# Optimization experiments

Hardware: AMD Instinct MI355X
Metric: run time of the kernel (lower is better)

Reference implementation:

```python
import jax, jax.numpy as jnp
import numpy as np

EPS = 1e-5


def layer_norm(x, g, b):
    m = jnp.mean(x, axis=-1, keepdims=True)
    v = jnp.mean((x - m) ** 2, axis=-1, keepdims=True)
    return (x - m) / jnp.sqrt(v + EPS) * g + b


def rel_shift(x, klen):
    # x: [q, p, b, n] -> Transformer-XL relative shift -> [q, klen, b, n]
    q, p, b, n = x.shape
    x = jnp.reshape(x, (p, q, b, n))
    x = x[1:]
    x = jnp.reshape(x, (q, p - 1, b, n))
    return x[:, :klen]


def setup_inputs() -> dict:
    S, B, D, NH, DH, DF = 1024, 4, 1024, 16, 64, 4096
    key = jax.random.key(0)
    ks = jax.random.split(key, 16)
    w = 0.02  # scale random params for numerical sanity
    return {
        "src": jax.random.normal(ks[0], (S, B, D), jnp.float32),
        "pos_emb": jax.random.normal(ks[1], (S + 1, B, D), jnp.float32),
        "src_mask": jnp.zeros((S, S), dtype=bool),
        "qw": jax.random.normal(ks[2], (D, NH, DH), jnp.float32) * w,
        "kw": jax.random.normal(ks[3], (D, NH, DH), jnp.float32) * w,
        "vw": jax.random.normal(ks[4], (D, NH, DH), jnp.float32) * w,
        "rw": jax.random.normal(ks[5], (D, NH, DH), jnp.float32) * w,
        "ow": jax.random.normal(ks[6], (D, NH, DH), jnp.float32) * w,
        "r_w_bias": jax.random.normal(ks[7], (NH, DH), jnp.float32) * w,
        "r_r_bias": jax.random.normal(ks[8], (NH, DH), jnp.float32) * w,
        "w1": jax.random.normal(ks[9], (DF, D), jnp.float32) * w,
        "b1": jnp.zeros((DF,), jnp.float32),
        "w2": jax.random.normal(ks[10], (D, DF), jnp.float32) * w,
        "b2": jnp.zeros((D,), jnp.float32),
        "g1": jnp.ones((D,), jnp.float32),
        "beta1": jnp.zeros((D,), jnp.float32),
        "g2": jnp.ones((D,), jnp.float32),
        "beta2": jnp.zeros((D,), jnp.float32),
    }


def reference(src, pos_emb, src_mask, qw, kw, vw, rw, ow, r_w_bias, r_r_bias,
              w1, b1, w2, b2, g1, beta1, g2, beta2):
    S = src.shape[0]
    d_head = qw.shape[-1]
    scale = 1.0 / d_head ** 0.5

    # mem=None -> cat == src; dropout layers are identity (eval)
    q_head = jnp.einsum('ibh,hnd->ibnd', src, qw)
    k_head = jnp.einsum('ibh,hnd->ibnd', src, kw)
    v_head = jnp.einsum('ibh,hnd->ibnd', src, vw)
    k_pos = jnp.einsum('ibh,hnd->ibnd', pos_emb, rw)

    ac = jnp.einsum('ibnd,jbnd->ijbn', q_head + r_w_bias, k_head)       # [S,S,B,N]
    bd = jnp.einsum('ibnd,jbnd->ijbn', q_head + r_r_bias, k_pos)        # [S,S+1,B,N]
    bd = rel_shift(bd, klen=S)

    mask = src_mask.astype(ac.dtype)[:, :, None, None]
    attn_score = (ac + bd) * scale - 1e30 * mask
    attn_prob = jax.nn.softmax(attn_score, axis=1)

    attn_vec = jnp.einsum('ijbn,jbnd->ibnd', attn_prob, v_head)
    attn_out = jnp.einsum('ibnd,hnd->ibh', attn_vec, ow)

    x = layer_norm(src + attn_out, g1, beta1)
    ff = jax.nn.gelu(x @ w1.T + b1, approximate=False) @ w2.T + b2
    return layer_norm(x + ff, g2, beta2)
```

## Files before the change

### kernel.cpp

```cpp
#include <hip/hip_runtime.h>
#include <math.h>

typedef __bf16 bf16x8 __attribute__((ext_vector_type(8)));
typedef __bf16 bf16x4 __attribute__((ext_vector_type(4)));
typedef float f32x4 __attribute__((ext_vector_type(4)));

__device__ __forceinline__ void gload_lds16(const __bf16* g, __bf16* l) {
  __builtin_amdgcn_global_load_lds((const __attribute__((address_space(1))) void*)g,
                                   (__attribute__((address_space(3))) void*)l, 16, 0, 0);
}

__device__ __forceinline__ float gelu_exact(float v) {
  return 0.5f * v * (1.f + erff(v * 0.70710678118654752f));
}

__global__ __launch_bounds__(256) void prep_all(
    const float* __restrict__ src, __bf16* __restrict__ srcB2,
    const float* __restrict__ pos, __bf16* __restrict__ posB,
    const float* __restrict__ ow, __bf16* __restrict__ owB,
    const float* __restrict__ w1, __bf16* __restrict__ w1B,
    const float* __restrict__ w2, __bf16* __restrict__ w2B,
    const float* __restrict__ qw, const float* __restrict__ kw,
    const float* __restrict__ vw, const float* __restrict__ rw,
    __bf16* __restrict__ qkvT, __bf16* __restrict__ rwT) {
  __shared__ float t[32][33];
  int bid = blockIdx.x;
  const int tid = threadIdx.x;
  if (bid < 4096) {
    const int i = bid & 1023, b = bid >> 10;
    const float4 v = *(const float4*)(src + ((size_t)(i * 4 + b)) * 1024 + tid * 4);
    bf16x4 o = {(__bf16)v.x, (__bf16)v.y, (__bf16)v.z, (__bf16)v.w};
    *(bf16x4*)(srcB2 + (size_t)bid * 1024 + tid * 4) = o;
    return;
  }
  bid -= 4096;
  if (bid < 3329) {
    const float* in; __bf16* out;
    if (bid < 1025) { in = pos; out = posB; }
    else if (bid < 1281) { bid -= 1025; in = ow; out = owB; }
    else if (bid < 2305) { bid -= 1281; in = w1; out = w1B; }
    else { bid -= 2305; in = w2; out = w2B; }
    const int base = bid * 4096 + tid * 4;
#pragma unroll
    for (int k2 = 0; k2 < 4; ++k2) {
      const int off = base + k2 * 1024;
      float4 v = *(const float4*)(in + off);
      bf16x4 o = {(__bf16)v.x, (__bf16)v.y, (__bf16)v.z, (__bf16)v.w};
      *(bf16x4*)(out + off) = o;
    }
    return;
  }
  bid -= 3329;
  const int z = bid >> 10, rem = bid & 1023;
  const float* in; __bf16* out;
  switch (z) {
    case 0: in = qw; out = qkvT; break;
    case 1: in = kw; out = qkvT + 1024 * 1024; break;
    case 2: in = vw; out = qkvT + 2048 * 1024; break;
    default: in = rw; out = rwT; break;
  }
  const int c0 = (rem & 31) * 32, r0 = (rem >> 5) * 32;
  const int tx = tid & 31, ty = tid >> 5;
  for (int yy = ty; yy < 32; yy += 8)
    t[yy][tx] = in[(size_t)(r0 + yy) * 1024 + c0 + tx];
  __syncthreads();
  for (int yy = ty; yy < 32; yy += 8)
    out[(size_t)(c0 + yy) * 1024 + r0 + tx] = (__bf16)t[tx][yy];
}

template<int BM, int BN, int MODE>
__device__ __forceinline__ void gemm_body(
    const __bf16* __restrict__ A, const __bf16* __restrict__ BT,
    float* __restrict__ Cf, __bf16* __restrict__ Cb,
    const float* __restrict__ bias, int M, int N, int K,
    int kStart, int kChunk, int mBase, int nBase, char* smemRaw) {
  constexpr int BK = 32;
  constexpr int ALOAD = (BM * BK) / 2048;
  constexpr int BLOAD = (BN * BK) / 2048;
  __bf16* lA = (__bf16*)smemRaw;
  __bf16* lB = (__bf16*)(smemRaw + 4 * BM * BK);
  const int tid = threadIdx.x;
  const int w = tid >> 6, l = tid & 63;
  const int lr = l & 15, lk = l >> 4;
  const int srow = tid >> 2;
  const int scol = (tid & 3) * 8;
  const int wbase = w * 512;

  const __bf16* aSrc[ALOAD];
  const __bf16* bSrc[BLOAD];
#pragma unroll
  for (int i = 0; i < ALOAD; ++i) {
    int grow = mBase + srow + i * 64;
    grow = grow < M ? grow : M - 1;
    aSrc[i] = A + (size_t)grow * K + kStart + scol;
  }
#pragma unroll
  for (int i = 0; i < BLOAD; ++i) {
    const int grow = nBase + srow + i * 64;
    bSrc[i] = BT + (size_t)grow * K + kStart + scol;
  }
  auto stage = [&](int buf) {
#pragma unroll
    for (int i = 0; i < ALOAD; ++i) {
      gload_lds16(aSrc[i], &lA[buf * BM * BK + i * 2048 + wbase]);
      aSrc[i] += BK;
    }
#pragma unroll
    for (int i = 0; i < BLOAD; ++i) {
      gload_lds16(bSrc[i], &lB[buf * BN * BK + i * 2048 + wbase]);
      bSrc[i] += BK;
    }
  };

  constexpr int WM = BM / 2, WN = BN / 2;
  constexpr int MF = WM / 16, NF = WN / 16;
  const int wr = w >> 1, wc = w & 1;
  f32x4 acc[MF][NF] = {};

  const int nIter = kChunk / BK;
  stage(0);
  int cur = 0;
#pragma unroll 1
  for (int t = 0; t < nIter; ++t) {
    __syncthreads();
    if (t + 1 < nIter) stage(cur ^ 1);
    bf16x8 af[MF], bfr[NF];
#pragma unroll
    for (int mi = 0; mi < MF; ++mi)
      af[mi] = *(const bf16x8*)&lA[cur * BM * BK + (wr * WM + mi * 16 + lr) * BK + lk * 8];
#pragma unroll
    for (int nj = 0; nj < NF; ++nj)
      bfr[nj] = *(const bf16x8*)&lB[cur * BN * BK + (wc * WN + nj * 16 + lr) * BK + lk * 8];
#pragma unroll
    for (int mi = 0; mi < MF; ++mi)
#pragma unroll
      for (int nj = 0; nj < NF; ++nj)
        acc[mi][nj] = __builtin_amdgcn_mfma_f32_16x16x32_bf16(af[mi], bfr[nj], acc[mi][nj], 0, 0, 0);
    cur ^= 1;
  }
#pragma unroll
  for (int mi = 0; mi < MF; ++mi) {
#pragma unroll
    for (int nj = 0; nj < NF; ++nj) {
      const int col = nBase + wc * WN + nj * 16 + lr;
      const int row0 = mBase + wr * WM + mi * 16 + lk * 4;
#pragma unroll
      for (int j = 0; j < 4; ++j) {
        const int row = row0 + j;
        if (row < M) {
          float v = acc[mi][nj][j];
          if constexpr (MODE == 1) {
            v = gelu_exact(v + bias[col]);
            Cb[(size_t)row * N + col] = (__bf16)v;
          } else if constexpr (MODE == 2) {
            Cb[(size_t)row * N + col] = (__bf16)v;
          } else {
            Cf[(size_t)row * N + col] = v;
          }
        }
      }
    }
  }
}

__global__ __launch_bounds__(256)
void proj2_kernel(const __bf16* __restrict__ vwT, const __bf16* __restrict__ srcB2,
                  const __bf16* __restrict__ posB, const __bf16* __restrict__ rwT,
                  __bf16* __restrict__ vTB, __bf16* __restrict__ kposB) {
  __shared__ __align__(16) char smem[4 * (128 + 64) * 32];
  const int raw = blockIdx.x;
  int bid = (raw & 7) * 130 + (raw >> 3);
  if (bid < 512) {
    gemm_body<128, 64, 2>(vwT, srcB2, nullptr, vTB, nullptr, 1024, 4096, 1024,
                          0, 1024, (bid >> 6) * 128, (bid & 63) * 64, smem);
  } else {
    const int t = bid - 512;
    gemm_body<128, 64, 2>(posB, rwT, nullptr, kposB, nullptr, 4100, 1024, 1024,
                          0, 1024, (t >> 4) * 128, (t & 15) * 64, smem);
  }
}

template<int MODE>
__global__ __launch_bounds__(512)
void gemm256(const __bf16* __restrict__ A, const __bf16* __restrict__ BT,
             __bf16* __restrict__ Cb, const float* __restrict__ bias,
             int M, int N, int K) {
  __shared__ __align__(16) __bf16 sm[3 * 24576];
  const int tid = threadIdx.x;
  const int wid = tid >> 6, l = tid & 63;
  const int lcol = l & 15, lk = l >> 4;
  const int wm = wid >> 1, wn = wid & 1;
  const int gx = gridDim.x;
  const int G = gx * gridDim.y;
  const int flat = blockIdx.y * gx + blockIdx.x;
  const int band = G >> 3;
  const int x8 = flat & 7, loc = flat >> 3;
  const int rpb = band / gx;
  const int ny = x8 * rpb + loc % rpb;
  const int nx = loc / rpb;
  const int mBase = ny * 256, nBase = nx * 128;

  int rowj[2], gslotj[2];
#pragma unroll
  for (int j = 0; j < 2; ++j) {
    const int u = (wid * 2 + j) * 64 + l;
    rowj[j] = u >> 3;
    gslotj[j] = (u & 7) ^ (rowj[j] & 7);
  }
  auto issueHT = [&](int kt, int ht, int side) {
    __bf16* base = sm + side * 24576 + (ht == 2 ? 16384 : ht * 8192);
#pragma unroll
    for (int j = 0; j < 2; ++j) {
      const __bf16* src = (ht < 2)
        ? A + (size_t)(mBase + ht * 128 + rowj[j]) * K + kt * 64 + gslotj[j] * 8
        : BT + (size_t)(nBase + rowj[j]) * K + kt * 64 + gslotj[j] * 8;
      gload_lds16(src, base + (wid * 2 + j) * 512);
    }
  };

  const int nkt = K >> 6;
  issueHT(0, 0, 0); issueHT(0, 1, 0); issueHT(0, 2, 0);
  issueHT(1, 0, 1); issueHT(1, 1, 1); issueHT(1, 2, 1);

  f32x4 acc[4][4] = {};
#pragma unroll 1
  for (int j = 0; j < nkt; ++j) {
    asm volatile("s_waitcnt vmcnt(6)" ::: "memory");
    __builtin_amdgcn_s_barrier();
    __builtin_amdgcn_sched_barrier(0);
    const int side = j % 3;
    const int sn = (j + 2) % 3;
    const int ktn = (j + 2 < nkt) ? j + 2 : nkt - 1;
    const __bf16* Ab = sm + side * 24576;
    const __bf16* Bb = Ab + 16384;
    issueHT(ktn, 0, sn);
    bf16x8 af[4][2];
#pragma unroll
    for (int mi = 0; mi < 4; ++mi)
#pragma unroll
      for (int kk = 0; kk < 2; ++kk) {
        const int row = wm * 64 + mi * 16 + lcol;
        af[mi][kk] = *(const bf16x8*)&Ab[row * 64 + (((kk * 4 + lk) ^ (row & 7)) * 8)];
      }
    issueHT(ktn, 1, sn);
    bf16x8 bfv[4][2];
#pragma unroll
    for (int nj = 0; nj < 4; ++nj)
#pragma unroll
      for (int kk = 0; kk < 2; ++kk) {
        const int row = wn * 64 + nj * 16 + lcol;
        bfv[nj][kk] = *(const bf16x8*)&Bb[row * 64 + (((kk * 4 + lk) ^ (row & 7)) * 8)];
      }
    issueHT(ktn, 2, sn);
    __builtin_amdgcn_s_setprio(1);
#pragma unroll
    for (int mi = 0; mi < 4; ++mi)
#pragma unroll
      for (int nj = 0; nj < 4; ++nj) {
        acc[mi][nj] = __builtin_amdgcn_mfma_f32_16x16x32_bf16(af[mi][0], bfv[nj][0], acc[mi][nj], 0, 0, 0);
        acc[mi][nj] = __builtin_amdgcn_mfma_f32_16x16x32_bf16(af[mi][1], bfv[nj][1], acc[mi][nj], 0, 0, 0);
      }
    __builtin_amdgcn_s_setprio(0);
  }
#pragma unroll
  for (int mi = 0; mi < 4; ++mi)
#pragma unroll
    for (int nj = 0; nj < 4; ++nj) {
      const int col = nBase + wn * 64 + nj * 16 + lcol;
      const int row0 = mBase + wm * 64 + mi * 16 + lk * 4;
#pragma unroll
      for (int jj = 0; jj < 4; ++jj) {
        float v = acc[mi][nj][jj];
        if constexpr (MODE == 1) v = gelu_exact(v + bias[col]);
        Cb[(size_t)(row0 + jj) * N + col] = (__bf16)v;
      }
    }
}

template<int MODE>
__global__ __launch_bounds__(512)
void gemm512(const __bf16* __restrict__ A, const __bf16* __restrict__ BT,
             __bf16* __restrict__ Cb0, __bf16* __restrict__ Cb1,
             __bf16* __restrict__ Cb2, __bf16* __restrict__ Cb3,
             const float* __restrict__ bias, int M, int N, int K, int kChunk) {
  __shared__ __align__(16) __bf16 sm[2 * 32768];
  const int tid = threadIdx.x;
  const int w = tid >> 6, l = tid & 63;
  const int lcol = l & 15, lk = l >> 4;
  const int wm = w >> 2, wn = w & 3;
  const int gx = gridDim.x;
  const int G = gx * gridDim.y;
  const int flat = blockIdx.y * gx + blockIdx.x;
  const int band = G >> 3;
  const int x8 = flat & 7, loc = flat >> 3;
  const int rpb = band / gx;
  const int ny = x8 * rpb + loc % rpb;
  const int nx = loc / rpb;
  const int mBase = ny * 256, nBase = nx * 256;
  const int kStart = blockIdx.z * kChunk;
  __bf16* Cb = (blockIdx.z == 0) ? Cb0 : (blockIdx.z == 1) ? Cb1
             : (blockIdx.z == 2) ? Cb2 : Cb3;

  const int rT = tid >> 3;
  const int gslot = ((tid & 7) ^ (rT & 7)) * 8;
  auto stage = [&](int side, int kt) {
#pragma unroll
    for (int i = 0; i < 4; ++i) {
      gload_lds16(A + (size_t)(mBase + i * 64 + rT) * K + kStart + kt * 64 + gslot,
                  sm + side * 32768 + i * 4096 + w * 512);
      gload_lds16(BT + (size_t)(nBase + i * 64 + rT) * K + kStart + kt * 64 + gslot,
                  sm + side * 32768 + 16384 + i * 4096 + w * 512);
    }
  };

  f32x4 acc[8][4] = {};
  const int nIter = kChunk >> 6;
  stage(0, 0);
  int cur = 0;
#pragma unroll 1
  for (int t = 0; t < nIter; ++t) {
    __syncthreads();
    if (t + 1 < nIter) stage(cur ^ 1, t + 1);
    const __bf16* Ab = sm + cur * 32768;
    const __bf16* Bb = Ab + 16384;
    bf16x8 bfv[4][2];
#pragma unroll
    for (int nj = 0; nj < 4; ++nj)
#pragma unroll
      for (int kk = 0; kk < 2; ++kk) {
        const int row = wn * 64 + nj * 16 + lcol;
        bfv[nj][kk] = *(const bf16x8*)&Bb[row * 64 + (((kk * 4 + lk) ^ (row & 7)) * 8)];
      }
    __builtin_amdgcn_s_setprio(1);
#pragma unroll
    for (int mi = 0; mi < 8; ++mi) {
      const int row = wm * 128 + mi * 16 + lcol;
      bf16x8 a0 = *(const bf16x8*)&Ab[row * 64 + ((lk ^ (row & 7)) * 8)];
      bf16x8 a1 = *(const bf16x8*)&Ab[row * 64 + (((4 + lk) ^ (row & 7)) * 8)];
#pragma unroll
      for (int nj = 0; nj < 4; ++nj) {
        acc[mi][nj] = __builtin_amdgcn_mfma_f32_16x16x32_bf16(a0, bfv[nj][0], acc[mi][nj], 0, 0, 0);
        acc[mi][nj] = __builtin_amdgcn_mfma_f32_16x16x32_bf16(a1, bfv[nj][1], acc[mi][nj], 0, 0, 0);
      }
    }
    __builtin_amdgcn_s_setprio(0);
    cur ^= 1;
  }
#pragma unroll
  for (int mi = 0; mi < 8; ++mi)
#pragma unroll
    for (int nj = 0; nj < 4; ++nj) {
      const int col = nBase + wn * 64 + nj * 16 + lcol;
      const int row0 = mBase + wm * 128 + mi * 16 + lk * 4;
#pragma unroll
      for (int jj = 0; jj < 4; ++jj) {
        float v = acc[mi][nj][jj];
        if constexpr (MODE == 1) v = gelu_exact(v + bias[col]);
        Cb[(size_t)(row0 + jj) * N + col] = (__bf16)v;
      }
    }
}

__global__ __launch_bounds__(256)
void attn11(const __bf16* __restrict__ qk, const __bf16* __restrict__ vT,
            const __bf16* __restrict__ kpos, const float* __restrict__ rwbias,
            const float* __restrict__ rrbias, __bf16* __restrict__ av) {
  constexpr float ALPHA = 0.125f * 1.44269504088896f;
  constexpr int PB = 132;
  __shared__ __align__(16) char smem[49664];
  __bf16* sK  = (__bf16*)(smem);
  __bf16* sKP = (__bf16*)(smem + 8192);
  __bf16* sVT = (__bf16*)(smem + 16384);
  __bf16* sP  = (__bf16*)(smem + 24576);
  __bf16* sbd = (__bf16*)(smem + 32768);

  const int flat = blockIdx.x;
  const int xcd = flat & 7, rr_ = flat >> 3;
  const int bn = xcd * 8 + (rr_ >> 4);
  const int it = rr_ & 15;
  const int b = bn >> 4, n = bn & 15;
  const int i0 = it * 64;
  const int tid = threadIdx.x;
  const int l = tid & 63;
  const int lcol = l & 15, lk = l >> 4;
  const int strip = (tid >> 6) * 16;
  const int wbase = tid & 192;
  const int nh64 = n * 64;
  const int q = strip + lcol;

  const int rB = tid >> 3;
  const int cs8 = ((tid & 7) ^ (rB & 7)) * 8;

  bf16x8 onesf;
#pragma unroll
  for (int u = 0; u < 8; ++u) onesf[u] = (__bf16)1.0f;

  bf16x8 qac[2], qlo[2], qhi[2];
  {
    const __bf16* qrow = qk + ((size_t)(b * 1024 + i0 + q)) * 2048 + nh64;
    int gH = i0 + q + 1; gH = gH < 1024 ? gH : 1023;
    const __bf16* qrowH = qk + ((size_t)(b * 1024 + gH)) * 2048 + nh64;
#pragma unroll
    for (int kk = 0; kk < 2; ++kk) {
      bf16x8 qv = *(const bf16x8*)(qrow + kk * 32 + lk * 8);
      bf16x8 qh = *(const bf16x8*)(qrowH + kk * 32 + lk * 8);
      const int dbase = nh64 + kk * 32 + lk * 8;
#pragma unroll
      for (int u = 0; u < 8; ++u) {
        const float rb = rrbias[dbase + u];
        qac[kk][u] = (__bf16)(((float)qv[u] + rwbias[dbase + u]) * ALPHA);
        qlo[kk][u] = (__bf16)(((float)qv[u] + rb) * ALPHA);
        qhi[kk][u] = (__bf16)(((float)qh[u] + rb) * ALPHA);
      }
    }
  }

#pragma unroll
  for (int kq = 0; kq < 2; ++kq) {
    const int r = kq * 32 + rB;
    const int dst = (kq * 256 + wbase) * 8;
    gload_lds16(kpos + ((size_t)((960 - i0 + r) * 4 + b)) * 1024 + nh64 + cs8, sP + dst);
    gload_lds16(qk + ((size_t)(b * 1024 + r)) * 2048 + 1024 + nh64 + cs8, sK + dst);
    const int rrel = r - i0;
    const int idx = (rrel <= 0) ? (1024 + rrel) : (rrel - 1);
    gload_lds16(kpos + ((size_t)(idx * 4 + b)) * 1024 + nh64 + cs8, sKP + dst);
    gload_lds16(vT + ((size_t)(nh64 + r)) * 4096 + b * 1024 + cs8, sVT + dst);
  }
  __syncthreads();
  {
    const __bf16* kpl = sP;
    const int colb0 = (-i0 - 64) & 127;
#pragma unroll
    for (int fb = 0; fb < 4; ++fb) {
      const int row = fb * 16 + lcol;
      f32x4 g = {};
#pragma unroll
      for (int kk = 0; kk < 2; ++kk) {
        bf16x8 a = *(const bf16x8*)&kpl[row * 64 + (((kk * 4 + lk) ^ (lcol & 7)) * 8)];
        g = __builtin_amdgcn_mfma_f32_16x16x32_bf16(a, qlo[kk], g, 0, 0, 0);
      }
      bf16x4 gw = {(__bf16)g[0], (__bf16)g[1], (__bf16)g[2], (__bf16)g[3]};
      *(bf16x4*)&sbd[q * PB + ((colb0 + fb * 16 + lk * 4) & 127)] = gw;
    }
  }
  __syncthreads();

  f32x4 oacc[4] = {};
  f32x4 zq = {};
  size_t kS = (size_t)(b * 1024 + 64 + rB) * 2048 + 1024 + nh64 + cs8;
  size_t vS = (size_t)(nh64 + rB) * 4096 + b * 1024 + 64 + cs8;

  auto jtStep = [&](int jt, const bf16x8 (&qg)[2], bool dofix) {
    const int d0 = jt * 64 - i0;
    bf16x8 rKr[2], rKPr[2], rVTr[2];
#pragma unroll
    for (int kq = 0; kq < 2; ++kq) {
      rKr[kq] = *(const bf16x8*)(qk + kS + kq * 65536);
      rVTr[kq] = *(const bf16x8*)(vT + vS + kq * 131072);
      const int rreln = d0 + 64 + kq * 32 + rB;
      const int idx = (rreln <= 0) ? (1024 + rreln) : (rreln - 1);
      rKPr[kq] = *(const bf16x8*)(kpos + ((size_t)(idx * 4 + b)) * 1024 + nh64 + cs8);
    }
    kS += 131072; vS += 64;
    {
      __builtin_amdgcn_s_setprio(1);
#pragma unroll
      for (int fb = 0; fb < 4; ++fb) {
        const int row = fb * 16 + lcol;
        f32x4 g = {};
        g = __builtin_amdgcn_mfma_f32_16x16x32_bf16(
            *(const bf16x8*)&sKP[row * 64 + ((lk ^ (lcol & 7)) * 8)], qg[0], g, 0, 0, 0);
        g = __builtin_amdgcn_mfma_f32_16x16x32_bf16(
            *(const bf16x8*)&sKP[row * 64 + (((4 + lk) ^ (lcol & 7)) * 8)], qg[1], g, 0, 0, 0);
        bf16x4 gw = {(__bf16)g[0], (__bf16)g[1], (__bf16)g[2], (__bf16)g[3]};
        *(bf16x4*)&sbd[q * PB + ((d0 + fb * 16 + lk * 4) & 127)] = gw;
      }
      __builtin_amdgcn_s_setprio(0);
      if (dofix) {
        const int cl = tid >> 2, part = tid & 3;
        const __bf16* qs = qk + ((size_t)(b * 1024 + i0 + cl)) * 2048 + nh64 + part * 16;
        bf16x8 a0 = *(const bf16x8*)qs;
        bf16x8 a1 = *(const bf16x8*)(qs + 8);
        bf16x8 k0 = *(const bf16x8*)&sKP[(2 * part) * 8];
        bf16x8 k1 = *(const bf16x8*)&sKP[(2 * part + 1) * 8];
        float s64 = 0.f;
#pragma unroll
        for (int u = 0; u < 8; ++u)
          s64 += ((float)a0[u] + rrbias[nh64 + part * 16 + u]) * (float)k0[u]
               + ((float)a1[u] + rrbias[nh64 + part * 16 + 8 + u]) * (float)k1[u];
        s64 += __shfl_xor(s64, 1, 64);
        s64 += __shfl_xor(s64, 2, 64);
        if (part == 0) sbd[cl * PB] = (__bf16)(s64 * ALPHA);
      }
    }
    f32x4 sc[4];
    __builtin_amdgcn_s_setprio(1);
#pragma unroll
    for (int fk = 0; fk < 4; ++fk) {
      const int row = fk * 16 + lcol;
      f32x4 a = {};
#pragma unroll
      for (int kk = 0; kk < 2; ++kk) {
        bf16x8 kf = *(const bf16x8*)&sK[row * 64 + (((kk * 4 + lk) ^ (lcol & 7)) * 8)];
        a = __builtin_amdgcn_mfma_f32_16x16x32_bf16(kf, qac[kk], a, 0, 0, 0);
      }
      sc[fk] = a;
    }
    __builtin_amdgcn_s_setprio(0);
    {
      const int rowb = q * PB;
      const int sb = d0 - q;
#pragma unroll
      for (int fk = 0; fk < 4; ++fk) {
        const int cb = sb + fk * 16 + lk * 4;
        float e0 = exp2f(sc[fk][0] + (float)sbd[rowb + ((cb) & 127)]);
        float e1 = exp2f(sc[fk][1] + (float)sbd[rowb + ((cb + 1) & 127)]);
        float e2 = exp2f(sc[fk][2] + (float)sbd[rowb + ((cb + 2) & 127)]);
        float e3 = exp2f(sc[fk][3] + (float)sbd[rowb + ((cb + 3) & 127)]);
        bf16x4 pw = {(__bf16)e0, (__bf16)e1, (__bf16)e2, (__bf16)e3};
        *(bf16x4*)&sP[q * 64 + (((fk * 2 + (lk >> 1)) ^ (q & 7)) * 8) + (lk & 1) * 4] = pw;
      }
    }
    __builtin_amdgcn_s_setprio(1);
#pragma unroll
    for (int kk = 0; kk < 2; ++kk) {
      bf16x8 pa = *(const bf16x8*)&sP[q * 64 + (((kk * 4 + lk) ^ (q & 7)) * 8)];
      zq = __builtin_amdgcn_mfma_f32_16x16x32_bf16(pa, onesf, zq, 0, 0, 0);
#pragma unroll
      for (int fd = 0; fd < 4; ++fd) {
        const int vrow = fd * 16 + lcol;
        bf16x8 bv = *(const bf16x8*)&sVT[vrow * 64 + (((kk * 4 + lk) ^ (lcol & 7)) * 8)];
        oacc[fd] = __builtin_amdgcn_mfma_f32_16x16x32_bf16(pa, bv, oacc[fd], 0, 0, 0);
      }
    }
    __builtin_amdgcn_s_setprio(0);
    __syncthreads();
#pragma unroll
    for (int kq = 0; kq < 2; ++kq) {
      const int dst = (kq * 256 + tid) * 8;
      *(bf16x8*)(sK + dst) = rKr[kq];
      *(bf16x8*)(sKP + dst) = rKPr[kq];
      *(bf16x8*)(sVT + dst) = rVTr[kq];
    }
    __syncthreads();
  };

#pragma unroll 1
  for (int jt = 0; jt < it; ++jt) jtStep(jt, qlo, false);
  jtStep(it, qhi, true);
#pragma unroll 1
  for (int jt = it + 1; jt < 16; ++jt) jtStep(jt, qhi, false);

#pragma unroll
  for (int jj = 0; jj < 4; ++jj) {
    const float rz = 1.f / zq[jj];
    const int ig = i0 + strip + lk * 4 + jj;
    __bf16* dst = av + ((size_t)(ig * 4 + b)) * 1024 + nh64;
#pragma unroll
    for (int fd = 0; fd < 4; ++fd)
      dst[fd * 16 + lcol] = (__bf16)(oacc[fd][jj] * rz);
  }
}

__global__ __launch_bounds__(256)
void ln_fuse(const float* __restrict__ A, const __bf16* __restrict__ Ab,
             const __bf16* __restrict__ P0, const __bf16* __restrict__ P1,
             const __bf16* __restrict__ P2, const __bf16* __restrict__ P3,
             const float* __restrict__ cb, const float* __restrict__ g,
             const float* __restrict__ be, float* __restrict__ oF,
             __bf16* __restrict__ oB) {
  const int row = blockIdx.x, t = threadIdx.x;
  const size_t base = (size_t)row * 1024 + t * 4;
  float x0, x1, x2, x3;
  if (A) {
    const float4 a = *(const float4*)(A + base);
    x0 = a.x; x1 = a.y; x2 = a.z; x3 = a.w;
  } else {
    const bf16x4 a = *(const bf16x4*)(Ab + base);
    x0 = (float)a[0]; x1 = (float)a[1]; x2 = (float)a[2]; x3 = (float)a[3];
  }
  const bf16x4 p0 = *(const bf16x4*)(P0 + base);
  const bf16x4 p1 = *(const bf16x4*)(P1 + base);
  const bf16x4 p2 = *(const bf16x4*)(P2 + base);
  const bf16x4 p3 = *(const bf16x4*)(P3 + base);
  x0 += (float)p0[0] + (float)p1[0] + (float)p2[0] + (float)p3[0];
  x1 += (float)p0[1] + (float)p1[1] + (float)p2[1] + (float)p3[1];
  x2 += (float)p0[2] + (float)p1[2] + (float)p2[2] + (float)p3[2];
  x3 += (float)p0[3] + (float)p1[3] + (float)p2[3] + (float)p3[3];
  if (cb) {
    const float4 c = *(const float4*)(cb + t * 4);
    x0 += c.x; x1 += c.y; x2 += c.z; x3 += c.w;
  }
  float s = x0 + x1 + x2 + x3;
  float qq = x0 * x0 + x1 * x1 + x2 * x2 + x3 * x3;
#pragma unroll
  for (int o = 1; o < 64; o <<= 1) { s += __shfl_xor(s, o, 64); qq += __shfl_xor(qq, o, 64); }
  __shared__ float ss[4], qs[4];
  if ((t & 63) == 0) { ss[t >> 6] = s; qs[t >> 6] = qq; }
  __syncthreads();
  s = ss[0] + ss[1] + ss[2] + ss[3];
  qq = qs[0] + qs[1] + qs[2] + qs[3];
  const float mean = s * (1.f / 1024.f);
  const float var = qq * (1.f / 1024.f) - mean * mean;
  const float rstd = rsqrtf(var + 1e-5f);
  const float4 gv = *(const float4*)(g + t * 4);
  const float4 bev = *(const float4*)(be + t * 4);
  const float y0 = (x0 - mean) * rstd * gv.x + bev.x;
  const float y1 = (x1 - mean) * rstd * gv.y + bev.y;
  const float y2 = (x2 - mean) * rstd * gv.z + bev.z;
  const float y3 = (x3 - mean) * rstd * gv.w + bev.w;
  if (oF) {
    float4 r = {y0, y1, y2, y3};
    *(float4*)(oF + base) = r;
  }
  if (oB) {
    bf16x4 o4 = {(__bf16)y0, (__bf16)y1, (__bf16)y2, (__bf16)y3};
    *(bf16x4*)(oB + base) = o4;
  }
}

extern "C" void kernel_launch(void* const* d_in, const int* in_sizes, int n_in,
                              void* d_out, int out_size, void* d_ws, size_t ws_size,
                              hipStream_t stream) {
  const float* src    = (const float*)d_in[0];
  const float* pos    = (const float*)d_in[1];
  const float* qw     = (const float*)d_in[3];
  const float* kw     = (const float*)d_in[4];
  const float* vw     = (const float*)d_in[5];
  const float* rw     = (const float*)d_in[6];
  const float* ow     = (const float*)d_in[7];
  const float* rwbias = (const float*)d_in[8];
  const float* rrbias = (const float*)d_in[9];
  const float* w1     = (const float*)d_in[10];
  const float* b1     = (const float*)d_in[11];
  const float* w2     = (const float*)d_in[12];
  const float* b2     = (const float*)d_in[13];
  const float* g1     = (const float*)d_in[14];
  const float* be1    = (const float*)d_in[15];
  const float* g2     = (const float*)d_in[16];
  const float* be2    = (const float*)d_in[17];
  float* out = (float*)d_out;

  char* p = (char*)d_ws;
  auto alloc = [&](size_t bytes) { char* r = p; p += (bytes + 255) & ~(size_t)255; return r; };
  __bf16* qkB   = (__bf16*)alloc(4096ull * 2048 * 2);
  __bf16* vTB   = (__bf16*)alloc(1024ull * 4096 * 2);
  __bf16* kposB = (__bf16*)alloc(4100ull * 1024 * 2);
  __bf16* avB   = (__bf16*)alloc(4096ull * 1024 * 2);
  __bf16* srcB2 = (__bf16*)alloc(4096ull * 1024 * 2);
  __bf16* posB  = (__bf16*)alloc(4100ull * 1024 * 2);
  float*  xF    = (float*)alloc(4096ull * 1024 * 4);
  __bf16* w2B   = (__bf16*)alloc(4096ull * 1024 * 2);
  __bf16* qkvT  = (__bf16*)alloc(3072ull * 1024 * 2);
  __bf16* rwT   = (__bf16*)alloc(1024ull * 1024 * 2);
  __bf16* owB   = (__bf16*)alloc(1024ull * 1024 * 2);
  __bf16* w1B   = (__bf16*)alloc(4096ull * 1024 * 2);
  __bf16* xB    = (__bf16*)alloc(4096ull * 1024 * 2);
  __bf16* gB   = qkB;
  __bf16* xS0  = (__bf16*)xF;
  __bf16* xS1  = (__bf16*)xF + 4194304;

  prep_all<<<11521, 256, 0, stream>>>(src, srcB2, pos, posB, ow, owB, w1, w1B,
                                      w2, w2B, qw, kw, vw, rw, qkvT, rwT);
  gemm256<2><<<dim3(16, 16), 512, 0, stream>>>(srcB2, qkvT, qkB, nullptr, 4096, 2048, 1024);
  proj2_kernel<<<1040, 256, 0, stream>>>(qkvT + 2048 * 1024, srcB2, posB, rwT, vTB, kposB);
  attn11<<<dim3(1024), 256, 0, stream>>>(qkB, vTB, kposB, rwbias, rrbias, avB);
  gemm512<2><<<dim3(4, 16, 4), 512, 0, stream>>>(avB, owB, srcB2, posB, xS0, xS1, nullptr, 4096, 1024, 1024, 256);
  ln_fuse<<<4096, 256, 0, stream>>>(src, nullptr, srcB2, posB, xS0, xS1, nullptr, g1, be1, nullptr, xB);
  gemm512<1><<<dim3(16, 16), 512, 0, stream>>>(xB, w1B, gB, nullptr, nullptr, nullptr, b1, 4096, 4096, 1024, 1024);
  gemm512<2><<<dim3(4, 16, 4), 512, 0, stream>>>(gB, w2B, avB, w1B, xS0, xS1, nullptr, 4096, 1024, 4096, 1024);
  ln_fuse<<<4096, 256, 0, stream>>>(nullptr, xB, avB, w1B, xS0, xS1, b2, g2, be2, out, nullptr);
  (void)in_sizes; (void)n_in; (void)out_size; (void)ws_size;
}
```

Baseline: 284.4 us.

## Split attention key range across two blocks and merge partial outputs

The attention kernel now launches twice as many blocks, each covering half of the key tiles. Each block writes unnormalized partial outputs and row sums to scratch buffers, and a new merge kernel adds the two partials and normalizes them. The aim is more parallelism and better CU occupancy, since 1024 blocks each ran 16 serial key steps. The cost is an extra kernel launch, extra global traffic for the partials, and duplicated Q/bias setup per block. The softmax appears to use no running max, so the partial sums can be added directly.

```diff
diff --git a/kernel.cpp b/kernel.cpp
--- a/kernel.cpp
+++ b/kernel.cpp
@@ -362,9 +362,11 @@
 }
 
 __global__ __launch_bounds__(256)
-void attn11(const __bf16* __restrict__ qk, const __bf16* __restrict__ vT,
+void attn12(const __bf16* __restrict__ qk, const __bf16* __restrict__ vT,
             const __bf16* __restrict__ kpos, const float* __restrict__ rwbias,
-            const float* __restrict__ rrbias, __bf16* __restrict__ av) {
+            const float* __restrict__ rrbias, __bf16* __restrict__ avP0,
+            __bf16* __restrict__ avP1, float* __restrict__ zP0,
+            float* __restrict__ zP1) {
   constexpr float ALPHA = 0.125f * 1.44269504088896f;
   constexpr int PB = 132;
   __shared__ __align__(16) char smem[49664];
@@ -380,6 +382,9 @@
   const int it = rr_ & 15;
   const int b = bn >> 4, n = bn & 15;
   const int i0 = it * 64;
+  const int half = blockIdx.y;
+  const int jt0s = half * 8;
+  const int j0p = jt0s * 64;
   const int tid = threadIdx.x;
   const int l = tid & 63;
   const int lcol = l & 15, lk = l >> 4;
@@ -415,40 +420,61 @@
     }
   }
 
+  auto colfix = [&](const __bf16* bandbuf) {
+    const int cl = tid >> 2, part = tid & 3;
+    const __bf16* qs = qk + ((size_t)(b * 1024 + i0 + cl)) * 2048 + nh64 + part * 16;
+    bf16x8 a0 = *(const bf16x8*)qs;
+    bf16x8 a1 = *(const bf16x8*)(qs + 8);
+    bf16x8 k0 = *(const bf16x8*)&bandbuf[(2 * part) * 8];
+    bf16x8 k1 = *(const bf16x8*)&bandbuf[(2 * part + 1) * 8];
+    float s64 = 0.f;
+#pragma unroll
+    for (int u = 0; u < 8; ++u)
+      s64 += ((float)a0[u] + rrbias[nh64 + part * 16 + u]) * (float)k0[u]
+           + ((float)a1[u] + rrbias[nh64 + part * 16 + 8 + u]) * (float)k1[u];
+    s64 += __shfl_xor(s64, 1, 64);
+    s64 += __shfl_xor(s64, 2, 64);
+    if (part == 0) sbd[cl * PB] = (__bf16)(s64 * ALPHA);
+  };
+
+  const int rrel0p = j0p - i0 - 64;
 #pragma unroll
   for (int kq = 0; kq < 2; ++kq) {
     const int r = kq * 32 + rB;
     const int dst = (kq * 256 + wbase) * 8;
-    gload_lds16(kpos + ((size_t)((960 - i0 + r) * 4 + b)) * 1024 + nh64 + cs8, sP + dst);
-    gload_lds16(qk + ((size_t)(b * 1024 + r)) * 2048 + 1024 + nh64 + cs8, sK + dst);
-    const int rrel = r - i0;
+    const int rrelb = rrel0p + r;
+    const int idxb = (rrelb <= 0) ? (1024 + rrelb) : (rrelb - 1);
+    gload_lds16(kpos + ((size_t)(idxb * 4 + b)) * 1024 + nh64 + cs8, sP + dst);
+    gload_lds16(qk + ((size_t)(b * 1024 + j0p + r)) * 2048 + 1024 + nh64 + cs8, sK + dst);
+    const int rrel = j0p - i0 + r;
     const int idx = (rrel <= 0) ? (1024 + rrel) : (rrel - 1);
     gload_lds16(kpos + ((size_t)(idx * 4 + b)) * 1024 + nh64 + cs8, sKP + dst);
-    gload_lds16(vT + ((size_t)(nh64 + r)) * 4096 + b * 1024 + cs8, sVT + dst);
+    gload_lds16(vT + ((size_t)(nh64 + r)) * 4096 + b * 1024 + j0p + cs8, sVT + dst);
   }
   __syncthreads();
   {
     const __bf16* kpl = sP;
-    const int colb0 = (-i0 - 64) & 127;
+    const bf16x8 pg0 = (rrel0p >= 0) ? qhi[0] : qlo[0];
+    const bf16x8 pg1 = (rrel0p >= 0) ? qhi[1] : qlo[1];
 #pragma unroll
     for (int fb = 0; fb < 4; ++fb) {
       const int row = fb * 16 + lcol;
       f32x4 g = {};
-#pragma unroll
-      for (int kk = 0; kk < 2; ++kk) {
-        bf16x8 a = *(const bf16x8*)&kpl[row * 64 + (((kk * 4 + lk) ^ (lcol & 7)) * 8)];
-        g = __builtin_amdgcn_mfma_f32_16x16x32_bf16(a, qlo[kk], g, 0, 0, 0);
-      }
+      g = __builtin_amdgcn_mfma_f32_16x16x32_bf16(
+          *(const bf16x8*)&kpl[row * 64 + ((lk ^ (lcol & 7)) * 8)], pg0, g, 0, 0, 0);
+      g = __builtin_amdgcn_mfma_f32_16x16x32_bf16(
+          *(const bf16x8*)&kpl[row * 64 + (((4 + lk) ^ (lcol & 7)) * 8)], pg1, g, 0, 0, 0);
       bf16x4 gw = {(__bf16)g[0], (__bf16)g[1], (__bf16)g[2], (__bf16)g[3]};
-      *(bf16x4*)&sbd[q * PB + ((colb0 + fb * 16 + lk * 4) & 127)] = gw;
-    }
+      *(bf16x4*)&sbd[q * PB + ((rrel0p + fb * 16 + lk * 4) & 127)] = gw;
+    }
+    if (rrel0p == 0) colfix(sP);
   }
   __syncthreads();
 
   f32x4 oacc[4] = {};
   f32x4 zq = {};
-  size_t kS = (size_t)(b * 1024 + 64 + rB) * 2048 + 1024 + nh64 + cs8;
-  size_t vS = (size_t)(nh64 + rB) * 4096 + b * 1024 + 64 + cs8;
+  size_t kS = (size_t)(b * 1024 + j0p + 64 + rB) * 2048 + 1024 + nh64 + cs8;
+  size_t vS = (size_t)(nh64 + rB) * 4096 + b * 1024 + j0p + 64 + cs8;
 
   auto jtStep = [&](int jt, const bf16x8 (&qg)[2], bool dofix) {
     const int d0 = jt * 64 - i0;
@@ -476,22 +502,7 @@
         *(bf16x4*)&sbd[q * PB + ((d0 + fb * 16 + lk * 4) & 127)] = gw;
       }
       __builtin_amdgcn_s_setprio(0);
-      if (dofix) {
-        const int cl = tid >> 2, part = tid & 3;
-        const __bf16* qs = qk + ((size_t)(b * 1024 + i0 + cl)) * 2048 + nh64 + part * 16;
-        bf16x8 a0 = *(const bf16x8*)qs;
-        bf16x8 a1 = *(const bf16x8*)(qs + 8);
-        bf16x8 k0 = *(const bf16x8*)&sKP[(2 * part) * 8];
-        bf16x8 k1 = *(const bf16x8*)&sKP[(2 * part + 1) * 8];
-        float s64 = 0.f;
-#pragma unroll
-        for (int u = 0; u < 8; ++u)
-          s64 += ((float)a0[u] + rrbias[nh64 + part * 16 + u]) * (float)k0[u]
-               + ((float)a1[u] + rrbias[nh64 + part * 16 + 8 + u]) * (float)k1[u];
-        s64 += __shfl_xor(s64, 1, 64);
-        s64 += __shfl_xor(s64, 2, 64);
-        if (part == 0) sbd[cl * PB] = (__bf16)(s64 * ALPHA);
-      }
+      if (dofix) colfix(sKP);
     }
     f32x4 sc[4];
     __builtin_amdgcn_s_setprio(1);
@@ -545,21 +556,44 @@
     __syncthreads();
   };
 
+  const int lo = jt0s, hi = jt0s + 8;
+  const int mid0 = (it < hi) ? it : hi;
 #pragma unroll 1
-  for (int jt = 0; jt < it; ++jt) jtStep(jt, qlo, false);
-  jtStep(it, qhi, true);
+  for (int jt = lo; jt < mid0; ++jt) jtStep(jt, qlo, false);
+  if (it >= lo && it < hi) jtStep(it, qhi, true);
+  const int hs = (it + 1 > lo) ? it + 1 : lo;
 #pragma unroll 1
-  for (int jt = it + 1; jt < 16; ++jt) jtStep(jt, qhi, false);
-
+  for (int jt = hs; jt < hi; ++jt) jtStep(jt, qhi, false);
+
+  __bf16* avP = half ? avP1 : avP0;
+  float* zP = half ? zP1 : zP0;
 #pragma unroll
   for (int jj = 0; jj < 4; ++jj) {
-    const float rz = 1.f / zq[jj];
     const int ig = i0 + strip + lk * 4 + jj;
-    __bf16* dst = av + ((size_t)(ig * 4 + b)) * 1024 + nh64;
+    const int row = ig * 4 + b;
+    __bf16* dst = avP + ((size_t)row) * 1024 + nh64;
 #pragma unroll
     for (int fd = 0; fd < 4; ++fd)
-      dst[fd * 16 + lcol] = (__bf16)(oacc[fd][jj] * rz);
-  }
+      dst[fd * 16 + lcol] = (__bf16)oacc[fd][jj];
+    if (lcol == 0) zP[row * 16 + n] = zq[jj];
+  }
+}
+
+__global__ __launch_bounds__(256)
+void merge_av(const __bf16* __restrict__ p0, const __bf16* __restrict__ p1,
+              const float* __restrict__ z0, const float* __restrict__ z1,
+              __bf16* __restrict__ av) {
+  const int row = blockIdx.x, t = threadIdx.x;
+  const int n = t >> 4;
+  const float rz = 1.f / (z0[row * 16 + n] + z1[row * 16 + n]);
+  const size_t base = (size_t)row * 1024 + t * 4;
+  const bf16x4 a = *(const bf16x4*)(p0 + base);
+  const bf16x4 c = *(const bf16x4*)(p1 + base);
+  bf16x4 o = {(__bf16)(((float)a[0] + (float)c[0]) * rz),
+              (__bf16)(((float)a[1] + (float)c[1]) * rz),
+              (__bf16)(((float)a[2] + (float)c[2]) * rz),
+              (__bf16)(((float)a[3] + (float)c[3]) * rz)};
+  *(bf16x4*)(av + base) = o;
 }
 
 __global__ __launch_bounds__(256)
@@ -659,12 +693,16 @@
   __bf16* gB   = qkB;
   __bf16* xS0  = (__bf16*)xF;
   __bf16* xS1  = (__bf16*)xF + 4194304;
+  float*  zP0  = (float*)rwT;
+  float*  zP1  = zP0 + 65536;
 
   prep_all<<<11521, 256, 0, stream>>>(src, srcB2, pos, posB, ow, owB, w1, w1B,
                                       w2, w2B, qw, kw, vw, rw, qkvT, rwT);
   gemm256<2><<<dim3(16, 16), 512, 0, stream>>>(srcB2, qkvT, qkB, nullptr, 4096, 2048, 1024);
   proj2_kernel<<<1040, 256, 0, stream>>>(qkvT + 2048 * 1024, srcB2, posB, rwT, vTB, kposB);
-  attn11<<<dim3(1024), 256, 0, stream>>>(qkB, vTB, kposB, rwbias, rrbias, avB);
+  attn12<<<dim3(1024, 2), 256, 0, stream>>>(qkB, vTB, kposB, rwbias, rrbias,
+                                            xS0, xS1, zP0, zP1);
+  merge_av<<<4096, 256, 0, stream>>>(xS0, xS1, zP0, zP1, avB);
   gemm512<2><<<dim3(4, 16, 4), 512, 0, stream>>>(avB, owB, srcB2, posB, xS0, xS1, nullptr, 4096, 1024, 1024, 256);
   ln_fuse<<<4096, 256, 0, stream>>>(src, nullptr, srcB2, posB, xS0, xS1, nullptr, g1, be1, nullptr, xB);
   gemm512<1><<<dim3(16, 16), 512, 0, stream>>>(xB, w1B, gB, nullptr, nullptr, nullptr, b1, 4096, 4096, 1024, 1024);
```

Measured after the change: 286.1 us. Within noise of the previous version (+0.6%).

## Merge QK projection GEMM into the V/kpos projection launch

Applied to the files above, without the earlier changes.

Removes the separate 256x128-tile QK projection kernel and folds that GEMM into the existing projection kernel as 1024 extra 128x64-tile blocks, so Q/K, V-transpose and k_pos projections run in one launch of 2064 blocks. The intent is to drop a launch and its tail, and let the three independent GEMMs fill the GPU together. In exchange, the QK GEMM now uses smaller tiles with a shallower pipeline than the tuned 512-thread kernel, which lowers data reuse per block.

```diff
diff --git a/kernel.cpp b/kernel.cpp
--- a/kernel.cpp
+++ b/kernel.cpp
@@ -164,117 +164,25 @@
 }
 
 __global__ __launch_bounds__(256)
-void proj2_kernel(const __bf16* __restrict__ vwT, const __bf16* __restrict__ srcB2,
-                  const __bf16* __restrict__ posB, const __bf16* __restrict__ rwT,
+void proj3_kernel(const __bf16* __restrict__ srcB2, const __bf16* __restrict__ qkvT,
+                  const __bf16* __restrict__ vwT, const __bf16* __restrict__ posB,
+                  const __bf16* __restrict__ rwT, __bf16* __restrict__ qkB,
                   __bf16* __restrict__ vTB, __bf16* __restrict__ kposB) {
   __shared__ __align__(16) char smem[4 * (128 + 64) * 32];
   const int raw = blockIdx.x;
-  int bid = (raw & 7) * 130 + (raw >> 3);
-  if (bid < 512) {
+  int bid = (raw & 7) * 258 + (raw >> 3);
+  if (bid < 1024) {
+    gemm_body<128, 64, 2>(srcB2, qkvT, nullptr, qkB, nullptr, 4096, 2048, 1024,
+                          0, 1024, (bid >> 5) * 128, (bid & 31) * 64, smem);
+  } else if (bid < 1536) {
+    const int t = bid - 1024;
     gemm_body<128, 64, 2>(vwT, srcB2, nullptr, vTB, nullptr, 1024, 4096, 1024,
-                          0, 1024, (bid >> 6) * 128, (bid & 63) * 64, smem);
+                          0, 1024, (t >> 6) * 128, (t & 63) * 64, smem);
   } else {
-    const int t = bid - 512;
+    const int t = bid - 1536;
     gemm_body<128, 64, 2>(posB, rwT, nullptr, kposB, nullptr, 4100, 1024, 1024,
                           0, 1024, (t >> 4) * 128, (t & 15) * 64, smem);
   }
-}
-
-template<int MODE>
-__global__ __launch_bounds__(512)
-void gemm256(const __bf16* __restrict__ A, const __bf16* __restrict__ BT,
-             __bf16* __restrict__ Cb, const float* __restrict__ bias,
-             int M, int N, int K) {
-  __shared__ __align__(16) __bf16 sm[3 * 24576];
-  const int tid = threadIdx.x;
-  const int wid = tid >> 6, l = tid & 63;
-  const int lcol = l & 15, lk = l >> 4;
-  const int wm = wid >> 1, wn = wid & 1;
-  const int gx = gridDim.x;
-  const int G = gx * gridDim.y;
-  const int flat = blockIdx.y * gx + blockIdx.x;
-  const int band = G >> 3;
-  const int x8 = flat & 7, loc = flat >> 3;
-  const int rpb = band / gx;
-  const int ny = x8 * rpb + loc % rpb;
-  const int nx = loc / rpb;
-  const int mBase = ny * 256, nBase = nx * 128;
-
-  int rowj[2], gslotj[2];
-#pragma unroll
-  for (int j = 0; j < 2; ++j) {
-    const int u = (wid * 2 + j) * 64 + l;
-    rowj[j] = u >> 3;
-    gslotj[j] = (u & 7) ^ (rowj[j] & 7);
-  }
-  auto issueHT = [&](int kt, int ht, int side) {
-    __bf16* base = sm + side * 24576 + (ht == 2 ? 16384 : ht * 8192);
-#pragma unroll
-    for (int j = 0; j < 2; ++j) {
-      const __bf16* src = (ht < 2)
-        ? A + (size_t)(mBase + ht * 128 + rowj[j]) * K + kt * 64 + gslotj[j] * 8
-        : BT + (size_t)(nBase + rowj[j]) * K + kt * 64 + gslotj[j] * 8;
-      gload_lds16(src, base + (wid * 2 + j) * 512);
-    }
-  };
-
-  const int nkt = K >> 6;
-  issueHT(0, 0, 0); issueHT(0, 1, 0); issueHT(0, 2, 0);
-  issueHT(1, 0, 1); issueHT(1, 1, 1); issueHT(1, 2, 1);
-
-  f32x4 acc[4][4] = {};
-#pragma unroll 1
-  for (int j = 0; j < nkt; ++j) {
-    asm volatile("s_waitcnt vmcnt(6)" ::: "memory");
-    __builtin_amdgcn_s_barrier();
-    __builtin_amdgcn_sched_barrier(0);
-    const int side = j % 3;
-    const int sn = (j + 2) % 3;
-    const int ktn = (j + 2 < nkt) ? j + 2 : nkt - 1;
-    const __bf16* Ab = sm + side * 24576;
-    const __bf16* Bb = Ab + 16384;
-    issueHT(ktn, 0, sn);
-    bf16x8 af[4][2];
-#pragma unroll
-    for (int mi = 0; mi < 4; ++mi)
-#pragma unroll
-      for (int kk = 0; kk < 2; ++kk) {
-        const int row = wm * 64 + mi * 16 + lcol;
-        af[mi][kk] = *(const bf16x8*)&Ab[row * 64 + (((kk * 4 + lk) ^ (row & 7)) * 8)];
-      }
-    issueHT(ktn, 1, sn);
-    bf16x8 bfv[4][2];
-#pragma unroll
-    for (int nj = 0; nj < 4; ++nj)
-#pragma unroll
-      for (int kk = 0; kk < 2; ++kk) {
-        const int row = wn * 64 + nj * 16 + lcol;
-        bfv[nj][kk] = *(const bf16x8*)&Bb[row * 64 + (((kk * 4 + lk) ^ (row & 7)) * 8)];
-      }
-    issueHT(ktn, 2, sn);
-    __builtin_amdgcn_s_setprio(1);
-#pragma unroll
-    for (int mi = 0; mi < 4; ++mi)
-#pragma unroll
-      for (int nj = 0; nj < 4; ++nj) {
-        acc[mi][nj] = __builtin_amdgcn_mfma_f32_16x16x32_bf16(af[mi][0], bfv[nj][0], acc[mi][nj], 0, 0, 0);
-        acc[mi][nj] = __builtin_amdgcn_mfma_f32_16x16x32_bf16(af[mi][1], bfv[nj][1], acc[mi][nj], 0, 0, 0);
-      }
-    __builtin_amdgcn_s_setprio(0);
-  }
-#pragma unroll
-  for (int mi = 0; mi < 4; ++mi)
-#pragma unroll
-    for (int nj = 0; nj < 4; ++nj) {
-      const int col = nBase + wn * 64 + nj * 16 + lcol;
-      const int row0 = mBase + wm * 64 + mi * 16 + lk * 4;
-#pragma unroll
-      for (int jj = 0; jj < 4; ++jj) {
-        float v = acc[mi][nj][jj];
-        if constexpr (MODE == 1) v = gelu_exact(v + bias[col]);
-        Cb[(size_t)(row0 + jj) * N + col] = (__bf16)v;
-      }
-    }
 }
 
 template<int MODE>
@@ -662,8 +570,8 @@
 
   prep_all<<<11521, 256, 0, stream>>>(src, srcB2, pos, posB, ow, owB, w1, w1B,
                                       w2, w2B, qw, kw, vw, rw, qkvT, rwT);
-  gemm256<2><<<dim3(16, 16), 512, 0, stream>>>(srcB2, qkvT, qkB, nullptr, 4096, 2048, 1024);
-  proj2_kernel<<<1040, 256, 0, stream>>>(qkvT + 2048 * 1024, srcB2, posB, rwT, vTB, kposB);
+  proj3_kernel<<<2064, 256, 0, stream>>>(srcB2, qkvT, qkvT + 2048 * 1024, posB,
+                                         rwT, qkB, vTB, kposB);
   attn11<<<dim3(1024), 256, 0, stream>>>(qkB, vTB, kposB, rwbias, rrbias, avB);
   gemm512<2><<<dim3(4, 16, 4), 512, 0, stream>>>(avB, owB, srcB2, posB, xS0, xS1, nullptr, 4096, 1024, 1024, 256);
   ln_fuse<<<4096, 256, 0, stream>>>(src, nullptr, srcB2, posB, xS0, xS1, nullptr, g1, be1, nullptr, xB);
```

Measured after the change: 286.4 us. About the same (+0.7%).
